# Kernel tuning notes

Measured on AMD Instinct MI355X. Metric: run time of the kernel, lower is better.

Reference implementation:

```python
import jax, jax.numpy as jnp
import numpy as np

B, C, H, W = 4, 64, 64, 64
CQK = C // 8


def setup_inputs() -> dict:
    key = jax.random.key(0)
    ks = jax.random.split(key, 4)
    x = jax.random.normal(ks[0], (B, C, H, W), dtype=jnp.float32)
    Wq = jax.random.normal(ks[1], (CQK, C), dtype=jnp.float32) * (1.0 / np.sqrt(C))
    bq = jnp.zeros((CQK,), dtype=jnp.float32)
    Wk = jax.random.normal(ks[2], (CQK, C), dtype=jnp.float32) * (1.0 / np.sqrt(C))
    bk = jnp.zeros((CQK,), dtype=jnp.float32)
    Wv = jax.random.normal(ks[3], (C, C), dtype=jnp.float32) * (1.0 / np.sqrt(C))
    bv = jnp.zeros((C,), dtype=jnp.float32)
    gamma = jnp.ones((1,), dtype=jnp.float32)
    return {"x": x, "Wq": Wq, "bq": bq, "Wk": Wk, "bk": bk,
            "Wv": Wv, "bv": bv, "gamma": gamma}


def reference(x, Wq, bq, Wk, bk, Wv, bv, gamma):
    b, c, h, w = x.shape
    n = h * w
    xf = x.reshape(b, c, n)                      # [B, C, N]
    # 1x1 convs == per-pixel linear over channels
    q = jnp.einsum('oc,bcn->bon', Wq, xf) + bq[:, None]   # [B, C/8, N]
    k = jnp.einsum('oc,bcn->bon', Wk, xf) + bk[:, None]   # [B, C/8, N]
    v = jnp.einsum('oc,bcn->bon', Wv, xf) + bv[:, None]   # [B, C, N]
    # attention_map[b,i,j] = <q[:, i], k[:, j]>; softmax over j
    attn = jax.nn.softmax(jnp.einsum('bci,bcj->bij', q, k), axis=-1)  # [B, N, N]
    # out[b,c,i] = sum_j v[b,c,j] * attn[b,i,j]  (bmm(V, attn^T))
    out = jnp.einsum('bcj,bij->bci', v, attn).reshape(b, c, h, w)
    return gamma * out + x
```

## Files before the change

kernel.cpp:

```cpp
#include <hip/hip_runtime.h>
#include <hip/hip_bf16.h>
#include <math.h>

#define NPIX 4096

typedef __attribute__((ext_vector_type(8))) short s8;
typedef __attribute__((ext_vector_type(16))) float f16v;

typedef __attribute__((address_space(1))) const void glob_cv;
typedef __attribute__((address_space(3))) void lds_v;

static __device__ __forceinline__ unsigned packbf2(float a, float b) {
    union { __hip_bfloat162 h; unsigned u; } x;
    x.h = __float22bfloat162_rn(make_float2(a, b));
    return x.u;
}
static __device__ __forceinline__ float fexp2(float x) {
#if __has_builtin(__builtin_amdgcn_exp2f)
    return __builtin_amdgcn_exp2f(x);
#else
    return exp2f(x);
#endif
}

static __device__ __forceinline__ void gl_lds16(const unsigned short* g,
                                                unsigned short* l, int lane) {
#if __has_builtin(__builtin_amdgcn_global_load_lds)
    __builtin_amdgcn_global_load_lds((glob_cv*)g, (lds_v*)l, 16, 0, 0);
#else
    *(uint4*)(l + lane * 8) = *(const uint4*)g;
#endif
}

static __device__ __forceinline__ void lane_swap(unsigned a, unsigned b, int lh,
                                                 unsigned &x, unsigned &y) {
#if __has_builtin(__builtin_amdgcn_permlane32_swap)
    auto r = __builtin_amdgcn_permlane32_swap((int)a, (int)b, false, false);
    x = (unsigned)r[0];
    y = (unsigned)r[1];
#else
    unsigned sa = __shfl_xor(a, 32), sb = __shfl_xor(b, 32);
    x = lh ? sb : a;
    y = lh ? b : sa;
#endif
}

__global__ __launch_bounds__(512) void prep_kernel(
    const float* __restrict__ x,
    const float* __restrict__ Wq, const float* __restrict__ bq,
    const float* __restrict__ Wk, const float* __restrict__ bk,
    __hip_bfloat16* __restrict__ qbf, __hip_bfloat16* __restrict__ kbf,
    __hip_bfloat16* __restrict__ xbf)
{
    __shared__ float Xp[64][65];
    __shared__ unsigned short Qs[64][8];
    int t = threadIdx.x;
    int p = t & 63;
    int g = t >> 6;
    int bid = blockIdx.x;
    int og = bid & 1;
    int n0 = ((bid >> 1) & 63) << 6;
    int b  = bid >> 7;

    const float* xb = x + ((size_t)b << 18);
    __hip_bfloat16* xbb = xbf + ((size_t)b << 18);
#pragma unroll
    for (int u = 0; u < 8; ++u) {
        int c = g + (u << 3);
        float v = xb[((size_t)c << 12) + n0 + p];
        Xp[c][p] = v;
        if ((og == 0) ? (u < 4) : (u >= 4))
            xbb[((size_t)c << 12) + n0 + p] = __float2bfloat16(v);
    }
    __syncthreads();

    const float* W  = og ? Wk : Wq;
    const float* bb = og ? bk : bq;
    const float* wr = W + g * 64;
    float acc = bb[g];
#pragma unroll
    for (int c = 0; c < 64; ++c) acc = fmaf(wr[c], Xp[c][p], acc);
    if (!og) acc *= 1.4426950408889634f;

    union { __hip_bfloat16 h; unsigned short u; } cv;
    cv.h = __float2bfloat16(acc);
    Qs[p][g] = cv.u;
    __syncthreads();

    if (t < 64) {
        __hip_bfloat16* dst = (og ? kbf : qbf) + ((size_t)(b * NPIX + n0 + t) << 3);
        *(s8*)dst = *(const s8*)&Qs[t][0];
    }
}

__global__ __launch_bounds__(512, 4) void flash_fused_kernel(
    const __hip_bfloat16* __restrict__ qbf, const __hip_bfloat16* __restrict__ kbf,
    const __hip_bfloat16* __restrict__ xbf,
    const float* __restrict__ Wv, const float* __restrict__ bv,
    const float* __restrict__ x, const float* __restrict__ gamma,
    float* __restrict__ out)
{
    __shared__ __align__(16) char pool[65536];

    int t = threadIdx.x;
    int w    = t >> 6;
    int lane = t & 63;
    int l32  = lane & 31;
    int lh   = lane >> 5;

    int bid  = blockIdx.x;
    int lbid = ((bid & 7) << 6) + (bid >> 3);
    int b  = lbid >> 7;
    int i0 = (lbid & 127) << 5;

    const s8 zero8 = {0, 0, 0, 0, 0, 0, 0, 0};

    s8 qf;
    {
        s8 qv = *(const s8*)(qbf + ((size_t)(b * NPIX + i0 + l32) << 3));
        qf = (lh == 0) ? qv : zero8;
    }

    f16v acc[2];
    f16v zero16;
#pragma unroll
    for (int r = 0; r < 16; ++r) { acc[0][r] = 0.f; acc[1][r] = 0.f; zero16[r] = 0.f; }
    float lsum = 0.f;

    const __hip_bfloat16* kb = kbf + ((size_t)(b * NPIX) << 3) + ((size_t)(w << 9) << 3);
    const unsigned short* xg = (const unsigned short*)xbf + ((size_t)b << 18);

    unsigned short* mybuf = (unsigned short*)pool + (w << 12);

    int l2 = lane >> 2, lg = lane & 3;
    int srcb[4];
#pragma unroll
    for (int u = 0; u < 4; ++u) {
        int row = (u << 4) + l2;
        srcb[u] = (row << 12) + (w << 9) + ((lg ^ ((row >> 1) & 3)) << 3);
    }
    int sw = (l32 >> 1) & 3;
    int o00 = (l32 << 5) + ((lh ^ sw) << 3);
    int o01 = (l32 << 5) + (((2 + lh) ^ sw) << 3);
    int o10 = ((32 + l32) << 5) + ((lh ^ sw) << 3);
    int o11 = ((32 + l32) << 5) + (((2 + lh) ^ sw) << 3);

#define STAGE(BO, N) do {                                                    \
        unsigned short* lb_ = mybuf + (BO);                                  \
        _Pragma("unroll")                                                    \
        for (int u_ = 0; u_ < 4; ++u_)                                       \
            gl_lds16(xg + srcb[u_] + ((N) << 5), lb_ + (u_ << 9), lane);     \
    } while (0)

#define WAITN(N) do {                                                        \
        asm volatile("s_waitcnt vmcnt(" #N ")" ::: "memory");                \
        __builtin_amdgcn_sched_barrier(0);                                   \
    } while (0)

#define BODY(BO, KF) do {                                                    \
        f16v sC = __builtin_amdgcn_mfma_f32_32x32x16_bf16(KF, qf, zero16, 0, 0, 0); \
        float e_[16];                                                        \
        _Pragma("unroll")                                                    \
        for (int r_ = 0; r_ < 16; ++r_) e_[r_] = fexp2(sC[r_]);              \
        _Pragma("unroll")                                                    \
        for (int r_ = 0; r_ < 16; ++r_) lsum += e_[r_];                      \
        unsigned P2[8];                                                      \
        _Pragma("unroll")                                                    \
        for (int s_ = 0; s_ < 8; ++s_) P2[s_] = packbf2(e_[2*s_], e_[2*s_+1]); \
        unsigned b00,b01,b02,b03,b10,b11,b12,b13;                            \
        lane_swap(P2[0], P2[2], lh, b00, b02);                               \
        lane_swap(P2[1], P2[3], lh, b01, b03);                               \
        lane_swap(P2[4], P2[6], lh, b10, b12);                               \
        lane_swap(P2[5], P2[7], lh, b11, b13);                               \
        union { unsigned u[4]; s8 v; } bf0, bf1;                             \
        bf0.u[0]=b00; bf0.u[1]=b01; bf0.u[2]=b02; bf0.u[3]=b03;              \
        bf1.u[0]=b10; bf1.u[1]=b11; bf1.u[2]=b12; bf1.u[3]=b13;              \
        const unsigned short* xb_ = mybuf + (BO);                            \
        s8 xa;                                                               \
        xa = *(const s8*)(xb_ + o00);                                        \
        acc[0] = __builtin_amdgcn_mfma_f32_32x32x16_bf16(xa, bf0.v, acc[0], 0, 0, 0); \
        xa = *(const s8*)(xb_ + o01);                                        \
        acc[0] = __builtin_amdgcn_mfma_f32_32x32x16_bf16(xa, bf1.v, acc[0], 0, 0, 0); \
        xa = *(const s8*)(xb_ + o10);                                        \
        acc[1] = __builtin_amdgcn_mfma_f32_32x32x16_bf16(xa, bf0.v, acc[1], 0, 0, 0); \
        xa = *(const s8*)(xb_ + o11);                                        \
        acc[1] = __builtin_amdgcn_mfma_f32_32x32x16_bf16(xa, bf1.v, acc[1], 0, 0, 0); \
    } while (0)

    s8 kfA = *(const s8*)(kb + ((size_t)l32 << 3));
    STAGE(0, 0);
    s8 kfB = *(const s8*)(kb + ((size_t)(32 + l32) << 3));
    STAGE(2048, 1);

    for (int n = 0; n < 14; n += 2) {
        WAITN(5);
        BODY(0, kfA);
        kfA = *(const s8*)(kb + ((size_t)(((n + 2) << 5) + l32) << 3));
        STAGE(0, n + 2);
        WAITN(5);
        BODY(2048, kfB);
        kfB = *(const s8*)(kb + ((size_t)(((n + 3) << 5) + l32) << 3));
        STAGE(2048, n + 3);
    }
    WAITN(5);
    BODY(0, kfA);
    WAITN(0);
    BODY(2048, kfB);
#undef BODY
#undef WAITN
#undef STAGE

    float* OshA = (float*)pool;
    float* OshB = (float*)(pool + 8704);
    float* Linv = (float*)(pool + 17408);
    float* bvs  = (float*)(pool + 17536);
    float* Wvs  = (float*)(pool + 17792);
    float* Lsh  = (float*)(pool + 34176);

    lsum += __shfl_xor(lsum, 32);
    __syncthreads();
    if (lh == 0) Lsh[w * 32 + l32] = lsum;

    float* Og = (w >> 2) ? OshB : OshA;
    for (int s = 0; s < 4; ++s) {
        __syncthreads();
        if ((w & 3) == s) {
#pragma unroll
            for (int cm = 0; cm < 2; ++cm)
#pragma unroll
                for (int r = 0; r < 16; ++r) {
                    int cc = cm * 32 + (r & 3) + 8 * (r >> 2) + 4 * lh;
                    float* p = Og + l32 * 68 + cc;
                    if (s == 0) *p = acc[cm][r];
                    else        *p += acc[cm][r];
                }
        }
    }
    __syncthreads();

    if (t < 32) {
        float lt = 0.f;
#pragma unroll
        for (int ww = 0; ww < 8; ++ww) lt += Lsh[ww * 32 + t];
        Linv[t] = 1.0f / lt;
    }
    if (t < 64) bvs[t] = bv[t];
    {
        const float4* wsrc = (const float4*)Wv;
        float4* wdst = (float4*)Wvs;
        wdst[t] = wsrc[t];
        wdst[t + 512] = wsrc[t + 512];
    }
    __syncthreads();

    {
        int i  = t & 31;
        int cg = t >> 5;
        float inv = Linv[i];
        float res[4] = {0.f, 0.f, 0.f, 0.f};
#pragma unroll 4
        for (int cb = 0; cb < 16; ++cb) {
            float4 oa = *(const float4*)(OshA + i * 68 + cb * 4);
            float4 ob = *(const float4*)(OshB + i * 68 + cb * 4);
            float4 o = make_float4(oa.x + ob.x, oa.y + ob.y, oa.z + ob.z, oa.w + ob.w);
#pragma unroll
            for (int k = 0; k < 4; ++k) {
                const float4 wv4 = *(const float4*)(Wvs + (cg * 4 + k) * 64 + cb * 4);
                res[k] = fmaf(wv4.x, o.x, fmaf(wv4.y, o.y, fmaf(wv4.z, o.z, fmaf(wv4.w, o.w, res[k]))));
            }
        }
        float g = gamma[0];
        const float* xr = x + ((size_t)b << 18) + i0;
        float* outp = out + ((size_t)b << 18) + i0;
#pragma unroll
        for (int k = 0; k < 4; ++k) {
            int cch = cg * 4 + k;
            float attn = fmaf(res[k], inv, bvs[cch]);
            size_t off = ((size_t)cch << 12) + i;
            outp[off] = fmaf(g, attn, xr[off]);
        }
    }
}

extern "C" void kernel_launch(void* const* d_in, const int* in_sizes, int n_in,
                              void* d_out, int out_size, void* d_ws, size_t ws_size,
                              hipStream_t stream) {
    const float* x     = (const float*)d_in[0];
    const float* Wq    = (const float*)d_in[1];
    const float* bq    = (const float*)d_in[2];
    const float* Wk    = (const float*)d_in[3];
    const float* bk    = (const float*)d_in[4];
    const float* Wv    = (const float*)d_in[5];
    const float* bv    = (const float*)d_in[6];
    const float* gamma = (const float*)d_in[7];
    float* out = (float*)d_out;

    __hip_bfloat16* qbf = (__hip_bfloat16*)d_ws;
    __hip_bfloat16* kbf = qbf + (size_t)4 * NPIX * 8;
    __hip_bfloat16* xbf = kbf + (size_t)4 * NPIX * 8;

    prep_kernel<<<512, 512, 0, stream>>>(x, Wq, bq, Wk, bk, qbf, kbf, xbf);
    flash_fused_kernel<<<512, 512, 0, stream>>>(qbf, kbf, xbf, Wv, bv, x, gamma, out);
}
```

Before: 99.84 us.

## Process two 32-query tiles per block to reuse staged X tiles

Result: no change. 100.3 us (+0.5%).

```diff
diff --git a/kernel.cpp b/kernel.cpp
--- a/kernel.cpp
+++ b/kernel.cpp
@@ -93,7 +93,7 @@
     }
 }
 
-__global__ __launch_bounds__(512, 4) void flash_fused_kernel(
+__global__ __launch_bounds__(512, 2) void flash_fused_kernel(
     const __hip_bfloat16* __restrict__ qbf, const __hip_bfloat16* __restrict__ kbf,
     const __hip_bfloat16* __restrict__ xbf,
     const float* __restrict__ Wv, const float* __restrict__ bv,
@@ -109,23 +109,27 @@
     int lh   = lane >> 5;
 
     int bid  = blockIdx.x;
-    int lbid = ((bid & 7) << 6) + (bid >> 3);
-    int b  = lbid >> 7;
-    int i0 = (lbid & 127) << 5;
+    int lbid = ((bid & 7) << 5) + (bid >> 3);
+    int b  = lbid >> 6;
+    int i0 = (lbid & 63) << 6;
 
     const s8 zero8 = {0, 0, 0, 0, 0, 0, 0, 0};
 
-    s8 qf;
+    s8 qf0, qf1;
     {
-        s8 qv = *(const s8*)(qbf + ((size_t)(b * NPIX + i0 + l32) << 3));
-        qf = (lh == 0) ? qv : zero8;
-    }
-
-    f16v acc[2];
-    f16v zero16;
-#pragma unroll
-    for (int r = 0; r < 16; ++r) { acc[0][r] = 0.f; acc[1][r] = 0.f; zero16[r] = 0.f; }
-    float lsum = 0.f;
+        s8 qv0 = *(const s8*)(qbf + ((size_t)(b * NPIX + i0 + l32) << 3));
+        s8 qv1 = *(const s8*)(qbf + ((size_t)(b * NPIX + i0 + 32 + l32) << 3));
+        qf0 = (lh == 0) ? qv0 : zero8;
+        qf1 = (lh == 0) ? qv1 : zero8;
+    }
+
+    f16v acc00, acc01, acc10, acc11, zero16;
+#pragma unroll
+    for (int r = 0; r < 16; ++r) {
+        acc00[r] = 0.f; acc01[r] = 0.f; acc10[r] = 0.f; acc11[r] = 0.f;
+        zero16[r] = 0.f;
+    }
+    float lsum0 = 0.f, lsum1 = 0.f;
 
     const __hip_bfloat16* kb = kbf + ((size_t)(b * NPIX) << 3) + ((size_t)(w << 9) << 3);
     const unsigned short* xg = (const unsigned short*)xbf + ((size_t)b << 18);
@@ -157,56 +161,72 @@
         __builtin_amdgcn_sched_barrier(0);                                   \
     } while (0)
 
-#define BODY(BO, KF) do {                                                    \
-        f16v sC = __builtin_amdgcn_mfma_f32_32x32x16_bf16(KF, qf, zero16, 0, 0, 0); \
+#define SM(SC, LS, P2) do {                                                  \
         float e_[16];                                                        \
         _Pragma("unroll")                                                    \
-        for (int r_ = 0; r_ < 16; ++r_) e_[r_] = fexp2(sC[r_]);              \
+        for (int r_ = 0; r_ < 16; ++r_) e_[r_] = fexp2((SC)[r_]);            \
         _Pragma("unroll")                                                    \
-        for (int r_ = 0; r_ < 16; ++r_) lsum += e_[r_];                      \
-        unsigned P2[8];                                                      \
+        for (int r_ = 0; r_ < 16; ++r_) (LS) += e_[r_];                      \
         _Pragma("unroll")                                                    \
-        for (int s_ = 0; s_ < 8; ++s_) P2[s_] = packbf2(e_[2*s_], e_[2*s_+1]); \
-        unsigned b00,b01,b02,b03,b10,b11,b12,b13;                            \
-        lane_swap(P2[0], P2[2], lh, b00, b02);                               \
-        lane_swap(P2[1], P2[3], lh, b01, b03);                               \
-        lane_swap(P2[4], P2[6], lh, b10, b12);                               \
-        lane_swap(P2[5], P2[7], lh, b11, b13);                               \
-        union { unsigned u[4]; s8 v; } bf0, bf1;                             \
-        bf0.u[0]=b00; bf0.u[1]=b01; bf0.u[2]=b02; bf0.u[3]=b03;              \
-        bf1.u[0]=b10; bf1.u[1]=b11; bf1.u[2]=b12; bf1.u[3]=b13;              \
+        for (int s_ = 0; s_ < 8; ++s_) (P2)[s_] = packbf2(e_[2*s_], e_[2*s_+1]); \
+    } while (0)
+
+#define MKBF(P2, BF0, BF1) do {                                              \
+        unsigned c0,c1,c2,c3,c4,c5,c6,c7;                                    \
+        lane_swap((P2)[0], (P2)[2], lh, c0, c2);                             \
+        lane_swap((P2)[1], (P2)[3], lh, c1, c3);                             \
+        lane_swap((P2)[4], (P2)[6], lh, c4, c6);                             \
+        lane_swap((P2)[5], (P2)[7], lh, c5, c7);                             \
+        (BF0).u[0]=c0; (BF0).u[1]=c1; (BF0).u[2]=c2; (BF0).u[3]=c3;          \
+        (BF1).u[0]=c4; (BF1).u[1]=c5; (BF1).u[2]=c6; (BF1).u[3]=c7;          \
+    } while (0)
+
+#define BODY2(BO, KF) do {                                                   \
+        f16v sC0 = __builtin_amdgcn_mfma_f32_32x32x16_bf16(KF, qf0, zero16, 0, 0, 0); \
+        f16v sC1 = __builtin_amdgcn_mfma_f32_32x32x16_bf16(KF, qf1, zero16, 0, 0, 0); \
+        union { unsigned u[4]; s8 v; } bfA0, bfA1, bfB0, bfB1;               \
+        { unsigned P2[8]; SM(sC0, lsum0, P2); MKBF(P2, bfA0, bfA1); }        \
+        { unsigned P2[8]; SM(sC1, lsum1, P2); MKBF(P2, bfB0, bfB1); }        \
         const unsigned short* xb_ = mybuf + (BO);                            \
         s8 xa;                                                               \
         xa = *(const s8*)(xb_ + o00);                                        \
-        acc[0] = __builtin_amdgcn_mfma_f32_32x32x16_bf16(xa, bf0.v, acc[0], 0, 0, 0); \
+        acc00 = __builtin_amdgcn_mfma_f32_32x32x16_bf16(xa, bfA0.v, acc00, 0, 0, 0); \
+        acc10 = __builtin_amdgcn_mfma_f32_32x32x16_bf16(xa, bfB0.v, acc10, 0, 0, 0); \
         xa = *(const s8*)(xb_ + o01);                                        \
-        acc[0] = __builtin_amdgcn_mfma_f32_32x32x16_bf16(xa, bf1.v, acc[0], 0, 0, 0); \
+        acc00 = __builtin_amdgcn_mfma_f32_32x32x16_bf16(xa, bfA1.v, acc00, 0, 0, 0); \
+        acc10 = __builtin_amdgcn_mfma_f32_32x32x16_bf16(xa, bfB1.v, acc10, 0, 0, 0); \
         xa = *(const s8*)(xb_ + o10);                                        \
-        acc[1] = __builtin_amdgcn_mfma_f32_32x32x16_bf16(xa, bf0.v, acc[1], 0, 0, 0); \
+        acc01 = __builtin_amdgcn_mfma_f32_32x32x16_bf16(xa, bfA0.v, acc01, 0, 0, 0); \
+        acc11 = __builtin_amdgcn_mfma_f32_32x32x16_bf16(xa, bfB0.v, acc11, 0, 0, 0); \
         xa = *(const s8*)(xb_ + o11);                                        \
-        acc[1] = __builtin_amdgcn_mfma_f32_32x32x16_bf16(xa, bf1.v, acc[1], 0, 0, 0); \
-    } while (0)
-
+        acc01 = __builtin_amdgcn_mfma_f32_32x32x16_bf16(xa, bfA1.v, acc01, 0, 0, 0); \
+        acc11 = __builtin_amdgcn_mfma_f32_32x32x16_bf16(xa, bfB1.v, acc11, 0, 0, 0); \
+    } while (0)
+
+    __builtin_amdgcn_sched_barrier(0);
     s8 kfA = *(const s8*)(kb + ((size_t)l32 << 3));
     STAGE(0, 0);
+    __builtin_amdgcn_sched_barrier(0);
     s8 kfB = *(const s8*)(kb + ((size_t)(32 + l32) << 3));
     STAGE(2048, 1);
 
     for (int n = 0; n < 14; n += 2) {
         WAITN(5);
-        BODY(0, kfA);
+        BODY2(0, kfA);
         kfA = *(const s8*)(kb + ((size_t)(((n + 2) << 5) + l32) << 3));
         STAGE(0, n + 2);
         WAITN(5);
-        BODY(2048, kfB);
+        BODY2(2048, kfB);
         kfB = *(const s8*)(kb + ((size_t)(((n + 3) << 5) + l32) << 3));
         STAGE(2048, n + 3);
     }
     WAITN(5);
-    BODY(0, kfA);
+    BODY2(0, kfA);
     WAITN(0);
-    BODY(2048, kfB);
-#undef BODY
+    BODY2(2048, kfB);
+#undef BODY2
+#undef MKBF
+#undef SM
 #undef WAITN
 #undef STAGE
 
@@ -217,43 +237,52 @@
     float* Wvs  = (float*)(pool + 17792);
     float* Lsh  = (float*)(pool + 34176);
 
-    lsum += __shfl_xor(lsum, 32);
+    lsum0 += __shfl_xor(lsum0, 32);
+    lsum1 += __shfl_xor(lsum1, 32);
     __syncthreads();
-    if (lh == 0) Lsh[w * 32 + l32] = lsum;
-
-    float* Og = (w >> 2) ? OshB : OshA;
-    for (int s = 0; s < 4; ++s) {
+
+    float g = gamma[0];
+    const float* xr = x + ((size_t)b << 18) + i0;
+    float* outp = out + ((size_t)b << 18) + i0;
+
+    auto epi = [&](f16v& a0, f16v& a1, float ls, int ih) {
+        if (ih) __syncthreads();
+        if (lh == 0) Lsh[w * 32 + l32] = ls;
+
+        float* Og = (w >> 2) ? OshB : OshA;
+        for (int s = 0; s < 4; ++s) {
+            __syncthreads();
+            if ((w & 3) == s) {
+#pragma unroll
+                for (int cm = 0; cm < 2; ++cm) {
+                    f16v& ac = cm ? a1 : a0;
+#pragma unroll
+                    for (int r = 0; r < 16; ++r) {
+                        int cc = cm * 32 + (r & 3) + 8 * (r >> 2) + 4 * lh;
+                        float* p = Og + l32 * 68 + cc;
+                        if (s == 0) *p = ac[r];
+                        else        *p += ac[r];
+                    }
+                }
+            }
+        }
         __syncthreads();
-        if ((w & 3) == s) {
-#pragma unroll
-            for (int cm = 0; cm < 2; ++cm)
-#pragma unroll
-                for (int r = 0; r < 16; ++r) {
-                    int cc = cm * 32 + (r & 3) + 8 * (r >> 2) + 4 * lh;
-                    float* p = Og + l32 * 68 + cc;
-                    if (s == 0) *p = acc[cm][r];
-                    else        *p += acc[cm][r];
-                }
-        }
-    }
-    __syncthreads();
-
-    if (t < 32) {
-        float lt = 0.f;
-#pragma unroll
-        for (int ww = 0; ww < 8; ++ww) lt += Lsh[ww * 32 + t];
-        Linv[t] = 1.0f / lt;
-    }
-    if (t < 64) bvs[t] = bv[t];
-    {
-        const float4* wsrc = (const float4*)Wv;
-        float4* wdst = (float4*)Wvs;
-        wdst[t] = wsrc[t];
-        wdst[t + 512] = wsrc[t + 512];
-    }
-    __syncthreads();
-
-    {
+
+        if (t < 32) {
+            float lt = 0.f;
+#pragma unroll
+            for (int ww = 0; ww < 8; ++ww) lt += Lsh[ww * 32 + t];
+            Linv[t] = 1.0f / lt;
+        }
+        if (ih == 0) {
+            if (t < 64) bvs[t] = bv[t];
+            const float4* wsrc = (const float4*)Wv;
+            float4* wdst = (float4*)Wvs;
+            wdst[t] = wsrc[t];
+            wdst[t + 512] = wsrc[t + 512];
+        }
+        __syncthreads();
+
         int i  = t & 31;
         int cg = t >> 5;
         float inv = Linv[i];
@@ -269,17 +298,17 @@
                 res[k] = fmaf(wv4.x, o.x, fmaf(wv4.y, o.y, fmaf(wv4.z, o.z, fmaf(wv4.w, o.w, res[k]))));
             }
         }
-        float g = gamma[0];
-        const float* xr = x + ((size_t)b << 18) + i0;
-        float* outp = out + ((size_t)b << 18) + i0;
 #pragma unroll
         for (int k = 0; k < 4; ++k) {
             int cch = cg * 4 + k;
             float attn = fmaf(res[k], inv, bvs[cch]);
-            size_t off = ((size_t)cch << 12) + i;
+            size_t off = ((size_t)cch << 12) + (ih << 5) + i;
             outp[off] = fmaf(g, attn, xr[off]);
         }
-    }
+    };
+
+    epi(acc00, acc01, lsum0, 0);
+    epi(acc10, acc11, lsum1, 1);
 }
 
 extern "C" void kernel_launch(void* const* d_in, const int* in_sizes, int n_in,
@@ -300,5 +329,5 @@
     __hip_bfloat16* xbf = kbf + (size_t)4 * NPIX * 8;
 
     prep_kernel<<<512, 512, 0, stream>>>(x, Wq, bq, Wk, bk, qbf, kbf, xbf);
-    flash_fused_kernel<<<512, 512, 0, stream>>>(qbf, kbf, xbf, Wv, bv, x, gamma, out);
-}
+    flash_fused_kernel<<<256, 512, 0, stream>>>(qbf, kbf, xbf, Wv, bv, x, gamma, out);
+}
```
